# Kernel tuning notes

Hardware: AMD Instinct MI355X
Metric: run time of the kernel (lower is better)

The kernel has to match this reference:

```python
import jax, jax.numpy as jnp
import numpy as np

B, L, D, H, DH, M = 2, 2048, 512, 8, 2048, 128  # batch, seq, d_model, heads, d_hidden, max_rel_pos
HD = D // H
EPS = 1e-5


def _ln(x, w, b):
    mu = jnp.mean(x, axis=-1, keepdims=True)
    var = jnp.mean((x - mu) ** 2, axis=-1, keepdims=True)
    return (x - mu) * jax.lax.rsqrt(var + EPS) * w + b


def setup_inputs() -> dict:
    key = jax.random.key(0)
    ks = jax.random.split(key, 8)
    s = 0.02  # init std for weights
    return {
        "x": jax.random.normal(ks[0], (B, L, D), jnp.float32),
        "ln1_w": jnp.ones((D,), jnp.float32),
        "ln1_b": jnp.zeros((D,), jnp.float32),
        "qkv_w": jax.random.normal(ks[1], (D, 3 * D), jnp.float32) * s,
        "qkv_b": jnp.zeros((3 * D,), jnp.float32),
        "out_w": jax.random.normal(ks[2], (D, D), jnp.float32) * s,
        "out_b": jnp.zeros((D,), jnp.float32),
        "rel_bias": jax.random.normal(ks[3], (H, 2 * M - 1), jnp.float32) * s,
        "gamma1": 1e-4 * jnp.ones((D,), jnp.float32),
        "ln2_w": jnp.ones((D,), jnp.float32),
        "ln2_b": jnp.zeros((D,), jnp.float32),
        "ffn_in_w": jax.random.normal(ks[4], (D, 2 * DH), jnp.float32) * s,
        "ffn_in_b": jnp.zeros((2 * DH,), jnp.float32),
        "ffn_out_w": jax.random.normal(ks[5], (DH, D), jnp.float32) * s,
        "ffn_out_b": jnp.zeros((D,), jnp.float32),
        "gamma2": 1e-4 * jnp.ones((D,), jnp.float32),
    }


def _forward(x, ln1_w, ln1_b, qkv_w, qkv_b, out_w, out_b, rel_bias, gamma1,
             ln2_w, ln2_b, ffn_in_w, ffn_in_b, ffn_out_w, ffn_out_b, gamma2):
    b, l, d = x.shape
    # --- PreNorm attention with T5-style relative position bias ---
    h = _ln(x, ln1_w, ln1_b)
    qkv = h @ qkv_w + qkv_b                           # [B, L, 3D]
    q, k, v = jnp.split(qkv, 3, axis=-1)
    q = q.reshape(b, l, H, HD)
    k = k.reshape(b, l, H, HD)
    v = v.reshape(b, l, H, HD)
    scale = 1.0 / jnp.sqrt(jnp.asarray(HD, x.dtype))
    scores = jnp.einsum("bqhd,bkhd->bhqk", q, k) * scale   # [B, H, L, L]
    # relative position bias: clip(i - j) indexed into learned table
    ctx = jnp.arange(l)[:, None] - jnp.arange(l)[None, :]
    ctx = jnp.clip(ctx, -(M - 1), M - 1) + (M - 1)          # [L, L] in [0, 2M-2]
    rel = rel_bias[:, ctx]                                  # [H, L, L]
    scores = scores + rel[None]
    attn = jax.nn.softmax(scores, axis=-1)
    o = jnp.einsum("bhqk,bkhd->bqhd", attn, v).reshape(b, l, d)
    o = o @ out_w + out_b
    x = x + o * gamma1                                      # LayerScale residual
    # --- PreNorm GEGLU FFN ---
    h2 = _ln(x, ln2_w, ln2_b)
    ab = h2 @ ffn_in_w + ffn_in_b                           # [B, L, 2*DH]
    a, bgate = jnp.split(ab, 2, axis=-1)
    f = jax.nn.gelu(bgate, approximate=False) * a
    f = f @ ffn_out_w + ffn_out_b
    x = x + f * gamma2
    return x, attn


def reference(x, ln1_w, ln1_b, qkv_w, qkv_b, out_w, out_b, rel_bias, gamma1,
              ln2_w, ln2_b, ffn_in_w, ffn_in_b, ffn_out_w, ffn_out_b, gamma2):
    return _forward(x, ln1_w, ln1_b, qkv_w, qkv_b, out_w, out_b, rel_bias, gamma1,
                    ln2_w, ln2_b, ffn_in_w, ffn_in_b, ffn_out_w, ffn_out_b, gamma2)
```

## Files before the change

kernel.cpp:

```cpp
#include <hip/hip_runtime.h>
#include <math.h>

typedef __attribute__((ext_vector_type(4))) float f32x4;
typedef __attribute__((ext_vector_type(8))) short bf16x8;
typedef __attribute__((ext_vector_type(4))) short s16x4;

#if __has_builtin(__builtin_amdgcn_exp2f)
#define EXP2(x) __builtin_amdgcn_exp2f(x)
#else
#define EXP2(x) exp2f(x)
#endif

__device__ __forceinline__ unsigned short f2bf(float f) {
  union { float f; unsigned u; } v; v.f = f;
  return (unsigned short)((v.u + 0x7fffu + ((v.u >> 16) & 1u)) >> 16);
}

__global__ void ln_kernel(const float* __restrict__ in, const float* __restrict__ w,
                          const float* __restrict__ b, float* __restrict__ out) {
  __shared__ float sh[4];
  const int t = threadIdx.x;
  const float* p = in + (size_t)blockIdx.x * 512;
  float a0 = p[t], a1 = p[t + 256];
  float s = a0 + a1;
#pragma unroll
  for (int o = 32; o; o >>= 1) s += __shfl_down(s, o);
  if ((t & 63) == 0) sh[t >> 6] = s;
  __syncthreads();
  s = sh[0] + sh[1] + sh[2] + sh[3];
  float mu = s * (1.0f / 512.0f);
  float d0 = a0 - mu, d1 = a1 - mu;
  float q = d0 * d0 + d1 * d1;
  __syncthreads();
#pragma unroll
  for (int o = 32; o; o >>= 1) q += __shfl_down(q, o);
  if ((t & 63) == 0) sh[t >> 6] = q;
  __syncthreads();
  q = sh[0] + sh[1] + sh[2] + sh[3];
  float rstd = rsqrtf(q * (1.0f / 512.0f) + 1e-5f);
  float* po = out + (size_t)blockIdx.x * 512;
  po[t]       = d0 * rstd * w[t] + b[t];
  po[t + 256] = d1 * rstd * w[t + 256] + b[t + 256];
}

__global__ void transpose_w(const float* __restrict__ in, unsigned short* __restrict__ out,
                            int ldi, int ldo, long ibs, long obs) {
  __shared__ float tile[32][33];
  const float* ip = in + (long)blockIdx.z * ibs;
  unsigned short* op = out + (long)blockIdx.z * obs;
  const int tx = threadIdx.x & 31;
  const int ty = threadIdx.x >> 5;
  const int n0 = blockIdx.x * 32, k0 = blockIdx.y * 32;
#pragma unroll
  for (int i = 0; i < 4; ++i)
    tile[ty + i * 8][tx] = ip[(size_t)(k0 + ty + i * 8) * ldi + n0 + tx];
  __syncthreads();
#pragma unroll
  for (int i = 0; i < 4; ++i)
    op[(size_t)(n0 + ty + i * 8) * ldo + k0 + tx] = f2bf(tile[tx][ty + i * 8]);
}

template <int WM, int WN, int TM, int TN, int EPI>
__global__ __launch_bounds__(256) void gemm_kernel(
    const float* __restrict__ A, const unsigned short* __restrict__ Bt,
    float* __restrict__ C, unsigned short* __restrict__ Cbf,
    int K, int lda, int ldb, int ldc,
    const float* __restrict__ bias, const float* __restrict__ resid,
    const float* __restrict__ gamma) {
  constexpr int BM = WM * TM * 16;
  constexpr int BN = WN * TN * 16;
  __shared__ short As[BM * 32];
  __shared__ short Bs[BN * 32];

  const int tid = threadIdx.x;
  const int m0 = blockIdx.y * BM, n0 = blockIdx.x * BN;
  const int w = tid >> 6, lane = tid & 63;
  const int wm = w / WN, wn = w % WN;
  const int lrow = lane & 15, lq = lane >> 4;

  f32x4 acc[TM][TN];
#pragma unroll
  for (int i = 0; i < TM; ++i)
#pragma unroll
    for (int j = 0; j < TN; ++j) acc[i][j] = (f32x4){0.f, 0.f, 0.f, 0.f};

  for (int k0 = 0; k0 < K; k0 += 32) {
    __syncthreads();
#pragma unroll
    for (int it = 0; it < (BM * 8) / 256; ++it) {
      int c = it * 256 + tid;
      int row = c >> 3, col = (c & 7) << 2;
      float4 v = *(const float4*)(A + (size_t)(m0 + row) * lda + k0 + col);
      s16x4 r = {(short)f2bf(v.x), (short)f2bf(v.y), (short)f2bf(v.z), (short)f2bf(v.w)};
      *(s16x4*)(As + row * 32 + col) = r;
    }
#pragma unroll
    for (int it = 0; it < (BN * 4) / 256; ++it) {
      int c = it * 256 + tid;
      int row = c >> 2, col = (c & 3) << 3;
      *(bf16x8*)(Bs + row * 32 + col) =
          *(const bf16x8*)(Bt + (size_t)(n0 + row) * ldb + k0 + col);
    }
    __syncthreads();

    bf16x8 af[TM], bf[TN];
#pragma unroll
    for (int mi = 0; mi < TM; ++mi)
      af[mi] = *(const bf16x8*)(As + (wm * TM * 16 + mi * 16 + lrow) * 32 + lq * 8);
#pragma unroll
    for (int nj = 0; nj < TN; ++nj)
      bf[nj] = *(const bf16x8*)(Bs + (wn * TN * 16 + nj * 16 + lrow) * 32 + lq * 8);
#pragma unroll
    for (int mi = 0; mi < TM; ++mi)
#pragma unroll
      for (int nj = 0; nj < TN; ++nj)
        acc[mi][nj] = __builtin_amdgcn_mfma_f32_16x16x32_bf16(af[mi], bf[nj], acc[mi][nj], 0, 0, 0);
  }

#pragma unroll
  for (int mi = 0; mi < TM; ++mi) {
#pragma unroll
    for (int nj = 0; nj < TN; ++nj) {
      int gm0 = m0 + wm * TM * 16 + mi * 16 + lq * 4;
      int gn = n0 + wn * TN * 16 + nj * 16 + lrow;
#pragma unroll
      for (int r = 0; r < 4; ++r) {
        int gm = gm0 + r;
        size_t idx = (size_t)gm * ldc + gn;
        float v = acc[mi][nj][r];
        if constexpr (EPI == 0) {
          C[idx] = v + bias[gn];
        } else if constexpr (EPI == 4) {
          float u = v + bias[gn];
          C[idx] = u;
          if (gn < 1024)
            Cbf[idx] = f2bf(gn < 512 ? u * 0.18033688011112042f : u);
        } else {
          C[idx] = resid[idx] + (v + bias[gn]) * gamma[gn];
        }
      }
    }
  }
}

__global__ __launch_bounds__(256) void ffn1_gate_kernel(
    const float* __restrict__ A, const unsigned short* __restrict__ Bt,
    float* __restrict__ F, const float* __restrict__ bias) {
  __shared__ short As[128 * 32];
  __shared__ short Bs[64 * 32];
  __shared__ short Bs2[64 * 32];

  const int tid = threadIdx.x;
  const int n0 = blockIdx.x * 64, m0 = blockIdx.y * 128;
  const int w = tid >> 6, lane = tid & 63;
  const int wm = w >> 1, wn = w & 1;
  const int lrow = lane & 15, lq = lane >> 4;

  f32x4 acca[4][2], accb[4][2];
#pragma unroll
  for (int i = 0; i < 4; ++i)
#pragma unroll
    for (int j = 0; j < 2; ++j) {
      acca[i][j] = (f32x4){0.f, 0.f, 0.f, 0.f};
      accb[i][j] = (f32x4){0.f, 0.f, 0.f, 0.f};
    }

  for (int k0 = 0; k0 < 512; k0 += 32) {
    __syncthreads();
#pragma unroll
    for (int it = 0; it < 4; ++it) {
      int c = it * 256 + tid;
      int row = c >> 3, col = (c & 7) << 2;
      float4 v = *(const float4*)(A + (size_t)(m0 + row) * 512 + k0 + col);
      s16x4 r = {(short)f2bf(v.x), (short)f2bf(v.y), (short)f2bf(v.z), (short)f2bf(v.w)};
      *(s16x4*)(As + row * 32 + col) = r;
    }
    {
      int row = tid >> 2, col = (tid & 3) << 3;
      *(bf16x8*)(Bs + row * 32 + col) =
          *(const bf16x8*)(Bt + (size_t)(n0 + row) * 512 + k0 + col);
      *(bf16x8*)(Bs2 + row * 32 + col) =
          *(const bf16x8*)(Bt + (size_t)(2048 + n0 + row) * 512 + k0 + col);
    }
    __syncthreads();

    bf16x8 af[4], ba[2], bb[2];
#pragma unroll
    for (int mi = 0; mi < 4; ++mi)
      af[mi] = *(const bf16x8*)(As + (wm * 64 + mi * 16 + lrow) * 32 + lq * 8);
#pragma unroll
    for (int nj = 0; nj < 2; ++nj) {
      ba[nj] = *(const bf16x8*)(Bs + (wn * 32 + nj * 16 + lrow) * 32 + lq * 8);
      bb[nj] = *(const bf16x8*)(Bs2 + (wn * 32 + nj * 16 + lrow) * 32 + lq * 8);
    }
#pragma unroll
    for (int mi = 0; mi < 4; ++mi)
#pragma unroll
      for (int nj = 0; nj < 2; ++nj) {
        acca[mi][nj] = __builtin_amdgcn_mfma_f32_16x16x32_bf16(af[mi], ba[nj], acca[mi][nj], 0, 0, 0);
        accb[mi][nj] = __builtin_amdgcn_mfma_f32_16x16x32_bf16(af[mi], bb[nj], accb[mi][nj], 0, 0, 0);
      }
  }

#pragma unroll
  for (int mi = 0; mi < 4; ++mi)
#pragma unroll
    for (int nj = 0; nj < 2; ++nj) {
      int gm0 = m0 + wm * 64 + mi * 16 + lq * 4;
      int gn = n0 + wn * 32 + nj * 16 + lrow;
#pragma unroll
      for (int r = 0; r < 4; ++r) {
        float a = acca[mi][nj][r] + bias[gn];
        float bg = accb[mi][nj][r] + bias[2048 + gn];
        float g = 0.5f * bg * (1.0f + erff(bg * 0.70710678118654752f));
        F[(size_t)(gm0 + r) * 2048 + gn] = g * a;
      }
    }
}

__global__ __launch_bounds__(256, 4) void attn_fused(
    const unsigned short* __restrict__ qkvbf, const unsigned short* __restrict__ vt,
    const float* __restrict__ rel, float* __restrict__ attn, float* __restrict__ o) {
  __shared__ __align__(16) float p_f32[4 * 16 * 64];
  __shared__ float erel[256];
  __shared__ float rsum[32];
  __shared__ float rinv[32];

  const int tid = threadIdx.x;
  const int flat = blockIdx.y * 64 + blockIdx.x;
  const int swz = (flat & 7) * 128 + (flat >> 3);
  const int bh = swz >> 6;
  const int m0 = (swz & 63) * 32;
  const int b = bh >> 3, h = bh & 7;

  const int w = tid >> 6, lane = tid & 63;
  const int wm = w >> 1, wn = w & 1;
  const int lrow = lane & 15, lq = lane >> 4;

  const unsigned short* qb = qkvbf + (size_t)(b * 2048) * 1536 + h * 64;
  const unsigned short* kb = qb + 512;
  const unsigned short* vb = vt + (size_t)bh * 64 * 2048;
  float* ab = attn + (size_t)bh * 2048 * 2048;
  const float* relh = rel + h * 255;

  if (tid < 32) rsum[tid] = 0.f;
  if (tid < 255) erel[tid] = __expf(relh[tid]);

  bf16x8 qf[2];
#pragma unroll
  for (int c = 0; c < 2; ++c)
    qf[c] = *(const bf16x8*)(qb + (size_t)(m0 + wm * 16 + lrow) * 1536 + c * 32 + lq * 8);

  const unsigned short* krow = kb + (size_t)(wn * 64 + lrow) * 1536 + lq * 8;
  const unsigned short* vrow = vb + (size_t)lrow * 2048 + wn * 64 + lq * 8;

  __syncthreads();

  float psum[4] = {0.f, 0.f, 0.f, 0.f};
  const int dbase = (m0 + wm * 16 + lq * 4) - (wn * 64 + lrow);
  for (int t = 0; t < 16; ++t) {
    const int kt0 = t * 128;
    f32x4 acc[4];
#pragma unroll
    for (int nj = 0; nj < 4; ++nj) acc[nj] = (f32x4){0.f, 0.f, 0.f, 0.f};
#pragma unroll
    for (int c = 0; c < 2; ++c) {
      bf16x8 kf[4];
#pragma unroll
      for (int nj = 0; nj < 4; ++nj)
        kf[nj] = *(const bf16x8*)(krow + (size_t)(kt0 + nj * 16) * 1536 + c * 32);
#pragma unroll
      for (int nj = 0; nj < 4; ++nj)
        acc[nj] = __builtin_amdgcn_mfma_f32_16x16x32_bf16(qf[c], kf[nj], acc[nj], 0, 0, 0);
    }
    const int Dt = m0 - kt0;
    if (Dt >= 256 || Dt <= -160) {
      float ec = erel[Dt >= 256 ? 254 : 0];
#pragma unroll
      for (int r = 0; r < 4; ++r) {
        float s = 0.f;
#pragma unroll
        for (int nj = 0; nj < 4; ++nj) s += EXP2(acc[nj][r]);
        psum[r] += ec * s;
      }
    } else {
#pragma unroll
      for (int nj = 0; nj < 4; ++nj) {
        int d0 = dbase - kt0 - nj * 16;
#pragma unroll
        for (int r = 0; r < 4; ++r) {
          int d = d0 + r;
          d = d < -127 ? -127 : (d > 127 ? 127 : d);
          psum[r] += EXP2(acc[nj][r]) * erel[d + 127];
        }
      }
    }
  }
#pragma unroll
  for (int off = 1; off < 16; off <<= 1)
#pragma unroll
    for (int r = 0; r < 4; ++r) psum[r] += __shfl_xor(psum[r], off);
  if (lrow == 0) {
#pragma unroll
    for (int r = 0; r < 4; ++r) atomicAdd(&rsum[wm * 16 + lq * 4 + r], psum[r]);
  }
  __syncthreads();
  if (tid < 32) rinv[tid] = 1.0f / rsum[tid];
  __syncthreads();
  float rv[4];
#pragma unroll
  for (int r = 0; r < 4; ++r) rv[r] = rinv[wm * 16 + lq * 4 + r];

  f32x4 oacc[4];
#pragma unroll
  for (int nj = 0; nj < 4; ++nj) oacc[nj] = (f32x4){0.f, 0.f, 0.f, 0.f};
  float* pw = p_f32 + w * (16 * 64);

  const int wsw = lq << 4;
  const int rsw = ((lrow >> 2) & 3) << 4;

  for (int t = 0; t < 16; ++t) {
    const int kt0 = t * 128;
    f32x4 acc[4];
#pragma unroll
    for (int nj = 0; nj < 4; ++nj) acc[nj] = (f32x4){0.f, 0.f, 0.f, 0.f};
#pragma unroll
    for (int c = 0; c < 2; ++c) {
      bf16x8 kf[4];
#pragma unroll
      for (int nj = 0; nj < 4; ++nj)
        kf[nj] = *(const bf16x8*)(krow + (size_t)(kt0 + nj * 16) * 1536 + c * 32);
#pragma unroll
      for (int nj = 0; nj < 4; ++nj)
        acc[nj] = __builtin_amdgcn_mfma_f32_16x16x32_bf16(qf[c], kf[nj], acc[nj], 0, 0, 0);
    }

    const int Dt = m0 - kt0;
    if (Dt >= 256 || Dt <= -160) {
      float ec = erel[Dt >= 256 ? 254 : 0];
#pragma unroll
      for (int r = 0; r < 4; ++r) {
        float fr = ec * rv[r];
        int prow = lq * 4 + r;
#pragma unroll
        for (int nj = 0; nj < 4; ++nj) {
          float e = EXP2(acc[nj][r]) * fr;
          pw[prow * 64 + ((nj * 16 + lrow) ^ wsw)] = e;
        }
      }
    } else {
#pragma unroll
      for (int r = 0; r < 4; ++r) {
        int prow = lq * 4 + r;
        int d0 = dbase - kt0 + r;
#pragma unroll
        for (int nj = 0; nj < 4; ++nj) {
          int d = d0 - nj * 16;
          d = d < -127 ? -127 : (d > 127 ? 127 : d);
          float e = EXP2(acc[nj][r]) * (erel[d + 127] * rv[r]);
          pw[prow * 64 + ((nj * 16 + lrow) ^ wsw)] = e;
        }
      }
    }

#pragma unroll
    for (int it = 0; it < 4; ++it) {
      int rr = lq * 4 + it;
      f32x4 vv = *(const f32x4*)(pw + rr * 64 + ((lrow * 4) ^ wsw));
      __builtin_nontemporal_store(
          vv, (f32x4*)(ab + (size_t)(m0 + wm * 16 + rr) * 2048 + kt0 + wn * 64 + lrow * 4));
    }

#pragma unroll
    for (int c2 = 0; c2 < 2; ++c2) {
      const float* pp = pw + lrow * 64 + ((c2 * 32 + lq * 8) ^ rsw);
      f32x4 pa = *(const f32x4*)pp;
      f32x4 pb = *(const f32x4*)(pp + 4);
      bf16x8 ap = {(short)f2bf(pa[0]), (short)f2bf(pa[1]), (short)f2bf(pa[2]), (short)f2bf(pa[3]),
                   (short)f2bf(pb[0]), (short)f2bf(pb[1]), (short)f2bf(pb[2]), (short)f2bf(pb[3])};
      bf16x8 bv[4];
#pragma unroll
      for (int nj = 0; nj < 4; ++nj)
        bv[nj] = *(const bf16x8*)(vrow + (size_t)(nj * 16) * 2048 + kt0 + c2 * 32);
#pragma unroll
      for (int nj = 0; nj < 4; ++nj)
        oacc[nj] = __builtin_amdgcn_mfma_f32_16x16x32_bf16(ap, bv[nj], oacc[nj], 0, 0, 0);
    }
  }

  __syncthreads();
  float* osc = p_f32;
  if (wn == 0) {
#pragma unroll
    for (int nj = 0; nj < 4; ++nj)
#pragma unroll
      for (int r = 0; r < 4; ++r)
        osc[(wm * 16 + lq * 4 + r) * 64 + nj * 16 + lrow] = oacc[nj][r];
  }
  __syncthreads();
  if (wn == 1) {
#pragma unroll
    for (int nj = 0; nj < 4; ++nj)
#pragma unroll
      for (int r = 0; r < 4; ++r) {
        int rr = m0 + wm * 16 + lq * 4 + r;
        float v = oacc[nj][r] + osc[(wm * 16 + lq * 4 + r) * 64 + nj * 16 + lrow];
        o[(size_t)(b * 2048 + rr) * 512 + h * 64 + nj * 16 + lrow] = v;
      }
  }
}

extern "C" void kernel_launch(void* const* d_in, const int* in_sizes, int n_in,
                              void* d_out, int out_size, void* d_ws, size_t ws_size,
                              hipStream_t stream) {
  (void)in_sizes; (void)n_in; (void)out_size; (void)ws_size;
  const float* x        = (const float*)d_in[0];
  const float* ln1_w    = (const float*)d_in[1];
  const float* ln1_b    = (const float*)d_in[2];
  const float* qkv_w    = (const float*)d_in[3];
  const float* qkv_b    = (const float*)d_in[4];
  const float* out_w    = (const float*)d_in[5];
  const float* out_b    = (const float*)d_in[6];
  const float* rel_bias = (const float*)d_in[7];
  const float* gamma1   = (const float*)d_in[8];
  const float* ln2_w    = (const float*)d_in[9];
  const float* ln2_b    = (const float*)d_in[10];
  const float* ffn_in_w = (const float*)d_in[11];
  const float* ffn_in_b = (const float*)d_in[12];
  const float* ffn_out_w  = (const float*)d_in[13];
  const float* ffn_out_b  = (const float*)d_in[14];
  const float* gamma2   = (const float*)d_in[15];

  float* x_out = (float*)d_out;
  float* attn  = x_out + (size_t)2 * 2048 * 512;

  float* ws  = (float*)d_ws;
  float* h   = ws;
  float* qkv = h + 2097152;
  float* o   = qkv + 6291456;
  float* x1  = o + 2097152;
  float* f   = x1 + 2097152;
  unsigned short* bt_qkv  = (unsigned short*)(f + 8388608);
  unsigned short* bt_out  = bt_qkv + 786432;
  unsigned short* bt_ffn1 = bt_out + 262144;
  unsigned short* bt_ffn2 = bt_ffn1 + 2097152;
  unsigned short* vt      = bt_ffn2 + 1048576;
  unsigned short* qkvbf   = (unsigned short*)f;

  transpose_w<<<dim3(48, 16, 1), 256, 0, stream>>>(qkv_w,     bt_qkv,  1536, 512,  0, 0);
  transpose_w<<<dim3(16, 16, 1), 256, 0, stream>>>(out_w,     bt_out,  512,  512,  0, 0);
  transpose_w<<<dim3(128, 16, 1), 256, 0, stream>>>(ffn_in_w, bt_ffn1, 4096, 512,  0, 0);
  transpose_w<<<dim3(16, 64, 1), 256, 0, stream>>>(ffn_out_w, bt_ffn2, 512,  2048, 0, 0);

  ln_kernel<<<4096, 256, 0, stream>>>(x, ln1_w, ln1_b, h);

  gemm_kernel<2, 2, 2, 4, 4><<<dim3(12, 64, 1), 256, 0, stream>>>(
      h, bt_qkv, qkv, qkvbf, 512, 512, 512, 1536, qkv_b, nullptr, nullptr);

  transpose_w<<<dim3(2, 64, 8), 256, 0, stream>>>(
      qkv + 1024, vt, 1536, 2048, 64, (long)64 * 2048);
  transpose_w<<<dim3(2, 64, 8), 256, 0, stream>>>(
      qkv + (size_t)2048 * 1536 + 1024, vt + (size_t)8 * 64 * 2048, 1536, 2048, 64,
      (long)64 * 2048);

  attn_fused<<<dim3(64, 16, 1), 256, 0, stream>>>(qkvbf, vt, rel_bias, attn, o);

  gemm_kernel<2, 2, 2, 4, 3><<<dim3(4, 64, 1), 256, 0, stream>>>(
      o, bt_out, x1, nullptr, 512, 512, 512, 512, out_b, x, gamma1);

  ln_kernel<<<4096, 256, 0, stream>>>(x1, ln2_w, ln2_b, h);

  ffn1_gate_kernel<<<dim3(32, 32, 1), 256, 0, stream>>>(h, bt_ffn1, f, ffn_in_b);

  gemm_kernel<2, 2, 2, 4, 3><<<dim3(4, 64, 1), 256, 0, stream>>>(
      f, bt_ffn2, x_out, nullptr, 2048, 2048, 2048, 512, ffn_out_b, x1, gamma2);
}
```

Baseline: 602.1 us.

## Store intermediate activations in bf16 and feed GEMMs bf16 operands directly

LayerNorm outputs, the attention output, and the GEGLU output are now written as bf16. The GEMM kernels load them directly with 16-byte vector loads instead of reading fp32 and converting in the inner loop. The QKV GEMM no longer writes fp32 copies of the Q and K columns. GEMM tiles are reshaped to a taller-M, narrower-N layout with adjusted grids. This cuts activation memory traffic and conversion work, at a small precision cost from rounding residual-path inputs to bf16 earlier.

```diff
diff --git a/kernel.cpp b/kernel.cpp
--- a/kernel.cpp
+++ b/kernel.cpp
@@ -17,7 +17,7 @@
 }
 
 __global__ void ln_kernel(const float* __restrict__ in, const float* __restrict__ w,
-                          const float* __restrict__ b, float* __restrict__ out) {
+                          const float* __restrict__ b, unsigned short* __restrict__ out) {
   __shared__ float sh[4];
   const int t = threadIdx.x;
   const float* p = in + (size_t)blockIdx.x * 512;
@@ -38,9 +38,9 @@
   __syncthreads();
   q = sh[0] + sh[1] + sh[2] + sh[3];
   float rstd = rsqrtf(q * (1.0f / 512.0f) + 1e-5f);
-  float* po = out + (size_t)blockIdx.x * 512;
-  po[t]       = d0 * rstd * w[t] + b[t];
-  po[t + 256] = d1 * rstd * w[t + 256] + b[t + 256];
+  unsigned short* po = out + (size_t)blockIdx.x * 512;
+  po[t]       = f2bf(d0 * rstd * w[t] + b[t]);
+  po[t + 256] = f2bf(d1 * rstd * w[t + 256] + b[t + 256]);
 }
 
 __global__ void transpose_w(const float* __restrict__ in, unsigned short* __restrict__ out,
@@ -61,8 +61,8 @@
 }
 
 template <int WM, int WN, int TM, int TN, int EPI>
-__global__ __launch_bounds__(256) void gemm_kernel(
-    const float* __restrict__ A, const unsigned short* __restrict__ Bt,
+__global__ __launch_bounds__(256) void gemm_bb(
+    const unsigned short* __restrict__ A, const unsigned short* __restrict__ Bt,
     float* __restrict__ C, unsigned short* __restrict__ Cbf,
     int K, int lda, int ldb, int ldc,
     const float* __restrict__ bias, const float* __restrict__ resid,
@@ -87,15 +87,14 @@
   for (int k0 = 0; k0 < K; k0 += 32) {
     __syncthreads();
 #pragma unroll
-    for (int it = 0; it < (BM * 8) / 256; ++it) {
+    for (int it = 0; it < BM / 64; ++it) {
       int c = it * 256 + tid;
-      int row = c >> 3, col = (c & 7) << 2;
-      float4 v = *(const float4*)(A + (size_t)(m0 + row) * lda + k0 + col);
-      s16x4 r = {(short)f2bf(v.x), (short)f2bf(v.y), (short)f2bf(v.z), (short)f2bf(v.w)};
-      *(s16x4*)(As + row * 32 + col) = r;
-    }
-#pragma unroll
-    for (int it = 0; it < (BN * 4) / 256; ++it) {
+      int row = c >> 2, col = (c & 3) << 3;
+      *(bf16x8*)(As + row * 32 + col) =
+          *(const bf16x8*)(A + (size_t)(m0 + row) * lda + k0 + col);
+    }
+#pragma unroll
+    for (int it = 0; it < BN / 64; ++it) {
       int c = it * 256 + tid;
       int row = c >> 2, col = (c & 3) << 3;
       *(bf16x8*)(Bs + row * 32 + col) =
@@ -132,9 +131,10 @@
           C[idx] = v + bias[gn];
         } else if constexpr (EPI == 4) {
           float u = v + bias[gn];
-          C[idx] = u;
           if (gn < 1024)
             Cbf[idx] = f2bf(gn < 512 ? u * 0.18033688011112042f : u);
+          else
+            C[idx] = u;
         } else {
           C[idx] = resid[idx] + (v + bias[gn]) * gamma[gn];
         }
@@ -144,8 +144,8 @@
 }
 
 __global__ __launch_bounds__(256) void ffn1_gate_kernel(
-    const float* __restrict__ A, const unsigned short* __restrict__ Bt,
-    float* __restrict__ F, const float* __restrict__ bias) {
+    const unsigned short* __restrict__ A, const unsigned short* __restrict__ Bt,
+    unsigned short* __restrict__ F, const float* __restrict__ bias) {
   __shared__ short As[128 * 32];
   __shared__ short Bs[64 * 32];
   __shared__ short Bs2[64 * 32];
@@ -168,15 +168,15 @@
   for (int k0 = 0; k0 < 512; k0 += 32) {
     __syncthreads();
 #pragma unroll
-    for (int it = 0; it < 4; ++it) {
+    for (int it = 0; it < 2; ++it) {
       int c = it * 256 + tid;
-      int row = c >> 3, col = (c & 7) << 2;
-      float4 v = *(const float4*)(A + (size_t)(m0 + row) * 512 + k0 + col);
-      s16x4 r = {(short)f2bf(v.x), (short)f2bf(v.y), (short)f2bf(v.z), (short)f2bf(v.w)};
-      *(s16x4*)(As + row * 32 + col) = r;
+      int row = c >> 2, col = (c & 3) << 3;
+      *(bf16x8*)(As + row * 32 + col) =
+          *(const bf16x8*)(A + (size_t)(m0 + row) * 512 + k0 + col);
     }
     {
-      int row = tid >> 2, col = (tid & 3) << 3;
+      int c = tid;
+      int row = c >> 2, col = (c & 3) << 3;
       *(bf16x8*)(Bs + row * 32 + col) =
           *(const bf16x8*)(Bt + (size_t)(n0 + row) * 512 + k0 + col);
       *(bf16x8*)(Bs2 + row * 32 + col) =
@@ -213,14 +213,14 @@
         float a = acca[mi][nj][r] + bias[gn];
         float bg = accb[mi][nj][r] + bias[2048 + gn];
         float g = 0.5f * bg * (1.0f + erff(bg * 0.70710678118654752f));
-        F[(size_t)(gm0 + r) * 2048 + gn] = g * a;
+        F[(size_t)(gm0 + r) * 2048 + gn] = f2bf(g * a);
       }
     }
 }
 
 __global__ __launch_bounds__(256, 4) void attn_fused(
     const unsigned short* __restrict__ qkvbf, const unsigned short* __restrict__ vt,
-    const float* __restrict__ rel, float* __restrict__ attn, float* __restrict__ o) {
+    const float* __restrict__ rel, float* __restrict__ attn, unsigned short* __restrict__ o) {
   __shared__ __align__(16) float p_f32[4 * 16 * 64];
   __shared__ float erel[256];
   __shared__ float rsum[32];
@@ -405,7 +405,7 @@
       for (int r = 0; r < 4; ++r) {
         int rr = m0 + wm * 16 + lq * 4 + r;
         float v = oacc[nj][r] + osc[(wm * 16 + lq * 4 + r) * 64 + nj * 16 + lrow];
-        o[(size_t)(b * 2048 + rr) * 512 + h * 64 + nj * 16 + lrow] = v;
+        o[(size_t)(b * 2048 + rr) * 512 + h * 64 + nj * 16 + lrow] = f2bf(v);
       }
   }
 }
@@ -435,27 +435,27 @@
   float* attn  = x_out + (size_t)2 * 2048 * 512;
 
   float* ws  = (float*)d_ws;
-  float* h   = ws;
-  float* qkv = h + 2097152;
-  float* o   = qkv + 6291456;
-  float* x1  = o + 2097152;
-  float* f   = x1 + 2097152;
-  unsigned short* bt_qkv  = (unsigned short*)(f + 8388608);
+  float* qkv = ws;
+  float* x1  = qkv + 6291456;
+  unsigned short* h_bf  = (unsigned short*)(x1 + 2097152);
+  unsigned short* o_bf  = h_bf + 2097152;
+  unsigned short* f_bf  = o_bf + 2097152;
+  unsigned short* qkvbf = f_bf;
+  unsigned short* bt_qkv  = f_bf + 8388608;
   unsigned short* bt_out  = bt_qkv + 786432;
   unsigned short* bt_ffn1 = bt_out + 262144;
   unsigned short* bt_ffn2 = bt_ffn1 + 2097152;
   unsigned short* vt      = bt_ffn2 + 1048576;
-  unsigned short* qkvbf   = (unsigned short*)f;
 
   transpose_w<<<dim3(48, 16, 1), 256, 0, stream>>>(qkv_w,     bt_qkv,  1536, 512,  0, 0);
   transpose_w<<<dim3(16, 16, 1), 256, 0, stream>>>(out_w,     bt_out,  512,  512,  0, 0);
   transpose_w<<<dim3(128, 16, 1), 256, 0, stream>>>(ffn_in_w, bt_ffn1, 4096, 512,  0, 0);
   transpose_w<<<dim3(16, 64, 1), 256, 0, stream>>>(ffn_out_w, bt_ffn2, 512,  2048, 0, 0);
 
-  ln_kernel<<<4096, 256, 0, stream>>>(x, ln1_w, ln1_b, h);
-
-  gemm_kernel<2, 2, 2, 4, 4><<<dim3(12, 64, 1), 256, 0, stream>>>(
-      h, bt_qkv, qkv, qkvbf, 512, 512, 512, 1536, qkv_b, nullptr, nullptr);
+  ln_kernel<<<4096, 256, 0, stream>>>(x, ln1_w, ln1_b, h_bf);
+
+  gemm_bb<2, 2, 4, 2, 4><<<dim3(24, 32, 1), 256, 0, stream>>>(
+      h_bf, bt_qkv, qkv, qkvbf, 512, 512, 512, 1536, qkv_b, nullptr, nullptr);
 
   transpose_w<<<dim3(2, 64, 8), 256, 0, stream>>>(
       qkv + 1024, vt, 1536, 2048, 64, (long)64 * 2048);
@@ -463,15 +463,15 @@
       qkv + (size_t)2048 * 1536 + 1024, vt + (size_t)8 * 64 * 2048, 1536, 2048, 64,
       (long)64 * 2048);
 
-  attn_fused<<<dim3(64, 16, 1), 256, 0, stream>>>(qkvbf, vt, rel_bias, attn, o);
-
-  gemm_kernel<2, 2, 2, 4, 3><<<dim3(4, 64, 1), 256, 0, stream>>>(
-      o, bt_out, x1, nullptr, 512, 512, 512, 512, out_b, x, gamma1);
-
-  ln_kernel<<<4096, 256, 0, stream>>>(x1, ln2_w, ln2_b, h);
-
-  ffn1_gate_kernel<<<dim3(32, 32, 1), 256, 0, stream>>>(h, bt_ffn1, f, ffn_in_b);
-
-  gemm_kernel<2, 2, 2, 4, 3><<<dim3(4, 64, 1), 256, 0, stream>>>(
-      f, bt_ffn2, x_out, nullptr, 2048, 2048, 2048, 512, ffn_out_b, x1, gamma2);
-}
+  attn_fused<<<dim3(64, 16, 1), 256, 0, stream>>>(qkvbf, vt, rel_bias, attn, o_bf);
+
+  gemm_bb<2, 2, 4, 2, 3><<<dim3(8, 32, 1), 256, 0, stream>>>(
+      o_bf, bt_out, x1, nullptr, 512, 512, 512, 512, out_b, x, gamma1);
+
+  ln_kernel<<<4096, 256, 0, stream>>>(x1, ln2_w, ln2_b, h_bf);
+
+  ffn1_gate_kernel<<<dim3(32, 32, 1), 256, 0, stream>>>(h_bf, bt_ffn1, f_bf, ffn_in_b);
+
+  gemm_bb<2, 2, 4, 2, 3><<<dim3(8, 32, 1), 256, 0, stream>>>(
+      f_bf, bt_ffn2, x_out, nullptr, 2048, 2048, 2048, 512, ffn_out_b, x1, gamma2);
+}
```

Measured after the change: 572.1 us. 1.05x faster.
